# Performance work log

Hardware: AMD Instinct MI355X
Metric: run time of the kernel (lower is better)

The kernel has to match this reference:

```python
import jax, jax.numpy as jnp
import numpy as np

N_TOKEN = 267735
CUTS = [0, 20000, 40000, 200000, 267735]
DIV = 4
D_MODEL = 1024
N_HEAD = 16
D_HEAD = 64
D_INNER = 4096
N_LAYER = 4
QLEN = 512
MLEN = 512
BSZ = 4
EPS = 1e-5


def _ln(x, g, b):
    mu = jnp.mean(x, axis=-1, keepdims=True)
    var = jnp.var(x, axis=-1, keepdims=True)
    return (x - mu) * jax.lax.rsqrt(var + EPS) * g + b


def _rel_shift(x):
    # x: [qlen, klen, bsz, n_head]
    q, k, b, n = x.shape
    x = jnp.pad(x, ((0, 0), (1, 0), (0, 0), (0, 0)))
    x = x.reshape(k + 1, q, b, n)[1:]
    return x.reshape(q, k, b, n)


def setup_inputs() -> dict:
    key = jax.random.key(0)
    ks = list(jax.random.split(key, 32))
    p = lambda i, shape: 0.02 * jax.random.normal(ks[i], shape, dtype=jnp.float32)
    inp = {}
    inp['input_ids'] = jax.random.randint(ks[0], (BSZ, QLEN), 0, N_TOKEN, dtype=jnp.int32)
    inp['mems'] = 0.05 * jax.random.normal(ks[1], (N_LAYER, MLEN, BSZ, D_MODEL), dtype=jnp.float32)
    # adaptive embedding: cluster tables + projections (div_val=4)
    for i in range(4):
        l, r = CUTS[i], CUTS[i + 1]
        d_i = D_MODEL // (DIV ** i)
        inp[f'emb{i}'] = p(2 + i, (r - l, d_i))
        inp[f'proj{i}'] = p(6 + i, (d_i, D_MODEL))
    H = N_HEAD * D_HEAD
    inp['qkv_W'] = p(10, (N_LAYER, D_MODEL, 3 * H))
    inp['r_W'] = p(11, (N_LAYER, D_MODEL, H))
    inp['o_W'] = p(12, (N_LAYER, H, D_MODEL))
    inp['r_w_bias'] = p(13, (N_LAYER, N_HEAD, D_HEAD))
    inp['r_r_bias'] = p(14, (N_LAYER, N_HEAD, D_HEAD))
    inp['ln1_g'] = jnp.ones((N_LAYER, D_MODEL), jnp.float32)
    inp['ln1_b'] = jnp.zeros((N_LAYER, D_MODEL), jnp.float32)
    inp['ff_w1'] = p(15, (N_LAYER, D_MODEL, D_INNER))
    inp['ff_b1'] = jnp.zeros((N_LAYER, D_INNER), jnp.float32)
    inp['ff_w2'] = p(16, (N_LAYER, D_INNER, D_MODEL))
    inp['ff_b2'] = jnp.zeros((N_LAYER, D_MODEL), jnp.float32)
    inp['ln2_g'] = jnp.ones((N_LAYER, D_MODEL), jnp.float32)
    inp['ln2_b'] = jnp.zeros((N_LAYER, D_MODEL), jnp.float32)
    return inp


def _forward(input_ids, mems, embs, projs, qkv_W, r_W, o_W, r_w_bias, r_r_bias,
             ln1_g, ln1_b, ff_w1, ff_b1, ff_w2, ff_b2, ln2_g, ln2_b):
    ids = input_ids.T  # [qlen, bsz]
    qlen, bsz = ids.shape
    mems = jax.lax.stop_gradient(mems)  # mems are detached in the original
    mlen = mems.shape[1]
    klen = qlen + mlen

    # --- adaptive embedding (masked gather + scatter-add, same math as boolean_mask/scatter_nd) ---
    flat = ids.reshape(-1)
    emb = jnp.zeros((flat.shape[0], D_MODEL), jnp.float32)
    for i in range(4):
        l, r = CUTS[i], CUTS[i + 1]
        mask = (flat >= l) & (flat < r)
        idx = jnp.clip(flat - l, 0, r - l - 1)
        e_i = jnp.einsum('id,de->ie', embs[i][idx], projs[i])
        emb = emb + jnp.where(mask[:, None], e_i, 0.0)
    word_emb = (emb * (D_MODEL ** 0.5)).reshape(qlen, bsz, D_MODEL)

    # --- sinusoidal relative positions, pos_seq = klen-1 .. 0 ---
    pos_seq = jnp.arange(klen - 1, -1, -1, dtype=jnp.float32)
    inv_freq = 1.0 / (10000.0 ** (jnp.arange(0, D_MODEL, 2, dtype=jnp.float32) / D_MODEL))
    sinusoid = jnp.einsum('i,j->ij', pos_seq, inv_freq)
    pos_emb = jnp.concatenate([jnp.sin(sinusoid), jnp.cos(sinusoid)], axis=-1)  # [klen, d_model]

    # causal mask over memory-extended keys: [qlen, klen]
    attn_mask = jnp.triu(jnp.ones((qlen, klen), jnp.float32), k=1 + mlen)
    mask4 = attn_mask[:, :, None, None]
    scale = 1.0 / (D_HEAD ** 0.5)

    h = word_emb
    for l in range(N_LAYER):
        cat = jnp.concatenate([mems[l], h], axis=0)  # [klen, bsz, d_model]
        w_heads = jnp.einsum('kbd,dh->kbh', cat, qkv_W[l])
        r_head_k = jnp.einsum('kd,dh->kh', pos_emb, r_W[l]).reshape(klen, N_HEAD, D_HEAD)
        q_h, k_h, v_h = jnp.split(w_heads, 3, axis=-1)
        q_h = q_h[-qlen:].reshape(qlen, bsz, N_HEAD, D_HEAD)
        k_h = k_h.reshape(klen, bsz, N_HEAD, D_HEAD)
        v_h = v_h.reshape(klen, bsz, N_HEAD, D_HEAD)
        AC = jnp.einsum('ibnd,jbnd->ijbn', q_h + r_w_bias[l], k_h)
        BD = _rel_shift(jnp.einsum('ibnd,jnd->ijbn', q_h + r_r_bias[l], r_head_k))
        score = (AC + BD) * scale
        score = score * (1.0 - mask4) - 1e30 * mask4
        prob = jax.nn.softmax(score, axis=1)
        attn_vec = jnp.einsum('ijbn,jbnd->ibnd', prob, v_h).reshape(qlen, bsz, N_HEAD * D_HEAD)
        attn_out = jnp.einsum('ibh,hd->ibd', attn_vec, o_W[l])
        h = _ln(h + attn_out, ln1_g[l], ln1_b[l])
        ff = jnp.einsum('ibf,fd->ibd', jax.nn.relu(jnp.einsum('ibd,df->ibf', h, ff_w1[l]) + ff_b1[l]), ff_w2[l]) + ff_b2[l]
        h = _ln(h + ff, ln2_g[l], ln2_b[l])

    return h.transpose(1, 0, 2)  # [bsz, qlen, d_model]


def reference(input_ids, mems, emb0, emb1, emb2, emb3, proj0, proj1, proj2, proj3,
              qkv_W, r_W, o_W, r_w_bias, r_r_bias, ln1_g, ln1_b,
              ff_w1, ff_b1, ff_w2, ff_b2, ln2_g, ln2_b):
    return _forward(input_ids, mems, (emb0, emb1, emb2, emb3), (proj0, proj1, proj2, proj3),
                    qkv_W, r_W, o_W, r_w_bias, r_r_bias, ln1_g, ln1_b,
                    ff_w1, ff_b1, ff_w2, ff_b2, ln2_g, ln2_b)
```

## Files before the change

kernel.cpp:

```cpp
#include <hip/hip_runtime.h>

typedef __attribute__((ext_vector_type(8))) short bf16x8;
typedef __attribute__((ext_vector_type(4))) float f32x4;

#define N_LAYER 4
#define QLEN 512
#define MLEN 512
#define KLEN 1024
#define BSZ 4
#define DM 1024
#define NH 16
#define DH 64
#define DINNER 4096
#define EK 1408
#define BDLD 1152

__device__ __forceinline__ unsigned short f2bf(float x) {
    unsigned u = __float_as_uint(x);
    u += 0x7fffu + ((u >> 16) & 1u);
    return (unsigned short)(u >> 16);
}
__device__ __forceinline__ float bf2f(unsigned short v) {
    return __uint_as_float(((unsigned)v) << 16);
}

__device__ __forceinline__ void gload16(const unsigned short* g, unsigned short* l) {
    __builtin_amdgcn_global_load_lds(
        (const __attribute__((address_space(1))) unsigned int*)g,
        (__attribute__((address_space(3))) unsigned int*)l, 16, 0, 0);
}

__device__ __forceinline__ bf16x8 lds_read8_sw(const unsigned short* base, int row, int cb) {
    return *(const bf16x8*)((const char*)base + row * 128 + (cb ^ ((row & 7) << 4)));
}

__global__ __launch_bounds__(256)
void transpose_all(const float* __restrict__ qkvWl, const float* __restrict__ rWl,
                   const float* __restrict__ oWl, const float* __restrict__ w1l,
                   const float* __restrict__ w2l,
                   unsigned short* __restrict__ qkvT, unsigned short* __restrict__ rT,
                   unsigned short* __restrict__ oT, unsigned short* __restrict__ w1T,
                   unsigned short* __restrict__ w2T) {
    __shared__ float tile[64][65];
    int id = blockIdx.x;
    const float* W; unsigned short* D; int K, N, bx, by;
    if (id < 768)       { W = qkvWl; D = qkvT; K = 1024; N = 3072; bx = id % 48; by = id / 48; }
    else if (id < 1024) { id -= 768;  W = rWl;  D = rT;  K = 1024; N = 1024; bx = id & 15; by = id >> 4; }
    else if (id < 1280) { id -= 1024; W = oWl;  D = oT;  K = 1024; N = 1024; bx = id & 15; by = id >> 4; }
    else if (id < 2304) { id -= 1280; W = w1l;  D = w1T; K = 1024; N = 4096; bx = id & 63; by = id >> 6; }
    else                { id -= 2304; W = w2l;  D = w2T; K = 4096; N = 1024; bx = id & 15; by = id >> 4; }
    const int tid = threadIdx.x;
#pragma unroll
    for (int s = 0; s < 4; ++s) {
        int idx = s * 256 + tid;
        int kr = idx >> 4, c4 = (idx & 15) * 4;
        float4 v = *(const float4*)(W + (size_t)(by * 64 + kr) * N + bx * 64 + c4);
        tile[kr][c4] = v.x; tile[kr][c4 + 1] = v.y;
        tile[kr][c4 + 2] = v.z; tile[kr][c4 + 3] = v.w;
    }
    __syncthreads();
#pragma unroll
    for (int s = 0; s < 2; ++s) {
        int idx = s * 256 + tid;
        int nl = idx >> 3, k8 = (idx & 7) * 8;
        unsigned short tmp[8];
#pragma unroll
        for (int j = 0; j < 8; ++j) tmp[j] = f2bf(tile[k8 + j][nl]);
        *(uint4*)(D + (size_t)(bx * 64 + nl) * K + by * 64 + k8) = *(uint4*)tmp;
    }
}

__global__ __launch_bounds__(256)
void transpose_pad(const float* __restrict__ W, unsigned short* __restrict__ dst,
                   int K, int N, int dstLD, int dstOff) {
    __shared__ float tile[32][33];
    const int tx = threadIdx.x & 31, ty = threadIdx.x >> 5;
    const int bx = blockIdx.x, by = blockIdx.y;
#pragma unroll
    for (int i = 0; i < 4; ++i) {
        int k = by * 32 + ty + i * 8;
        tile[ty + i * 8][tx] = (k < K) ? W[(size_t)k * N + bx * 32 + tx] : 0.f;
    }
    __syncthreads();
#pragma unroll
    for (int i = 0; i < 4; ++i) {
        int n = bx * 32 + ty + i * 8;
        int k = by * 32 + tx;
        dst[(size_t)n * dstLD + dstOff + k] = f2bf(tile[tx][ty + i * 8]);
    }
}

__global__ __launch_bounds__(256)
void emb_gather(const int* __restrict__ ids,
                const float* __restrict__ e0, const float* __restrict__ e1,
                const float* __restrict__ e2, const float* __restrict__ e3,
                unsigned short* __restrict__ embA) {
    const int chunk = blockIdx.x * 256 + threadIdx.x;
    if (chunk >= 2048 * 176) return;
    const int t = chunk / 176;
    const int e8 = (chunk - t * 176) * 8;
    const int i = t >> 2, b = t & 3;
    const int id = ids[b * QLEN + i];
    const float* src = nullptr;
    if (e8 < 1024) {
        if (id < 20000) src = e0 + (size_t)id * 1024 + e8;
    } else if (e8 < 1280) {
        if (id >= 20000 && id < 40000) src = e1 + (size_t)(id - 20000) * 256 + (e8 - 1024);
    } else if (e8 < 1344) {
        if (id >= 40000 && id < 200000) src = e2 + (size_t)(id - 40000) * 64 + (e8 - 1280);
    } else if (e8 < 1360) {
        if (id >= 200000) src = e3 + (size_t)(id - 200000) * 16 + (e8 - 1344);
    }
    uint4 o = {0u, 0u, 0u, 0u};
    if (src) {
        float4 v0 = *(const float4*)src;
        float4 v1 = *(const float4*)(src + 4);
        o.x = (unsigned)f2bf(v0.x * 32.f) | ((unsigned)f2bf(v0.y * 32.f) << 16);
        o.y = (unsigned)f2bf(v0.z * 32.f) | ((unsigned)f2bf(v0.w * 32.f) << 16);
        o.z = (unsigned)f2bf(v1.x * 32.f) | ((unsigned)f2bf(v1.y * 32.f) << 16);
        o.w = (unsigned)f2bf(v1.z * 32.f) | ((unsigned)f2bf(v1.w * 32.f) << 16);
    }
    *(uint4*)(embA + (size_t)t * EK + e8) = o;
}

template <int MODE, int BN>
__global__ __launch_bounds__(256)
void gemm_bt(const unsigned short* __restrict__ A, const unsigned short* __restrict__ BT,
             float* __restrict__ C, unsigned short* __restrict__ Cbf,
             const float* __restrict__ bias, int M, int N, int K) {
    constexpr int NF = BN / 32;
    __shared__ unsigned short lA[2][128 * 64];
    __shared__ unsigned short lB[2][BN * 64];
    const int tid = threadIdx.x;
    const int w = tid >> 6, l = tid & 63;
    const int lane15 = l & 15, lh = l >> 4;
    const int nwg = gridDim.x;
    const int cpx = nwg >> 3;
    const int swz = (blockIdx.x & 7) * cpx + (blockIdx.x >> 3);
    const int nbn = N / BN;
    const int bm = swz / nbn, bn = swz % nbn;
    const int wr = (w >> 1) * 64, wc = (w & 1) * (BN / 2);

    f32x4 acc[4][NF] = {};

    const unsigned short* gA = A + (size_t)(bm * 128) * K;
    const unsigned short* gB = BT + (size_t)(bn * BN) * K;

    auto stage = [&](int buf, int k0) {
#pragma unroll
        for (int s = 0; s < 4; ++s) {
            int g = tid + s * 256, row = g >> 3;
            gload16(gA + (size_t)row * K + k0 + ((g & 7) ^ (row & 7)) * 8,
                    lA[buf] + g * 8);
        }
#pragma unroll
        for (int s = 0; s < BN / 32; ++s) {
            int g = tid + s * 256, row = g >> 3;
            gload16(gB + (size_t)row * K + k0 + ((g & 7) ^ (row & 7)) * 8,
                    lB[buf] + g * 8);
        }
    };

    stage(0, 0);
    __syncthreads();
    int cur = 0;
    for (int k0 = 0; k0 < K; k0 += 64) {
        if (k0 + 64 < K) stage(cur ^ 1, k0 + 64);
        const unsigned short* cA = lA[cur];
        const unsigned short* cB = lB[cur];
#pragma unroll
        for (int kk = 0; kk < 2; ++kk) {
            bf16x8 af[4], bfr[NF];
#pragma unroll
            for (int f = 0; f < 4; ++f)
                af[f] = lds_read8_sw(cA, wr + f * 16 + lane15, kk * 64 + lh * 16);
#pragma unroll
            for (int f = 0; f < NF; ++f)
                bfr[f] = lds_read8_sw(cB, wc + f * 16 + lane15, kk * 64 + lh * 16);
#pragma unroll
            for (int mi = 0; mi < 4; ++mi)
#pragma unroll
                for (int ni = 0; ni < NF; ++ni)
                    acc[mi][ni] = __builtin_amdgcn_mfma_f32_16x16x32_bf16(
                        af[mi], bfr[ni], acc[mi][ni], 0, 0, 0);
        }
        __syncthreads();
        cur ^= 1;
    }

#pragma unroll
    for (int mi = 0; mi < 4; ++mi) {
        int rowb = bm * 128 + wr + mi * 16 + lh * 4;
#pragma unroll
        for (int ni = 0; ni < NF; ++ni) {
            int col = bn * BN + wc + ni * 16 + lane15;
#pragma unroll
            for (int r = 0; r < 4; ++r) {
                float x = acc[mi][ni][r];
                if (MODE == 0) {
                    C[(size_t)(rowb + r) * N + col] = x;
                } else if (MODE == 1) {
                    x += bias[col];
                    Cbf[(size_t)(rowb + r) * N + col] = f2bf(x > 0.f ? x : 0.f);
                } else if (MODE == 2) {
                    C[(size_t)(rowb + r) * N + col] = x + bias[col];
                } else {
                    C[(size_t)(rowb + r) * N + col] = x;
                    Cbf[(size_t)(rowb + r) * N + col] = f2bf(x);
                }
            }
        }
    }
}

__global__ __launch_bounds__(256)
void qkv_rk_gemm(const unsigned short* __restrict__ catb, const unsigned short* __restrict__ posb,
                 const unsigned short* __restrict__ qkvT, const unsigned short* __restrict__ rT,
                 const float* __restrict__ rwb, const float* __restrict__ rrb,
                 unsigned short* __restrict__ Qw, unsigned short* __restrict__ Qr,
                 unsigned short* __restrict__ Kb, unsigned short* __restrict__ VTb,
                 unsigned short* __restrict__ Rb) {
    __shared__ unsigned short lA[2][128 * 64];
    __shared__ unsigned short lB[2][128 * 64];
    const int tid = threadIdx.x;
    const int w = tid >> 6, l = tid & 63;
    const int lane15 = l & 15, lh = l >> 4;
    const int cpx = gridDim.x >> 3;
    const int swz = (blockIdx.x & 7) * cpx + (blockIdx.x >> 3);
    const int wr = (w >> 1) * 64, wc = (w & 1) * 64;

    const unsigned short* gA;
    const unsigned short* gB;
    int part, bm, bn;
    if (swz < 512)      { part = 0; bm = swz >> 4; bn = swz & 15;
                          gA = catb + (size_t)(bm * 128) * 1024;
                          gB = qkvT + (size_t)(1024 + bn * 128) * 1024; }
    else if (swz < 640) { part = 1; int q = swz - 512; bm = q >> 3; bn = q & 7;
                          gA = catb + (size_t)(2048 + bm * 128) * 1024;
                          gB = qkvT + (size_t)(bn * 128) * 1024; }
    else                { part = 2; int q = swz - 640; bm = q >> 3; bn = q & 7;
                          gA = posb + (size_t)(bm * 128) * 1024;
                          gB = rT + (size_t)(bn * 128) * 1024; }

    f32x4 acc[4][4] = {};
    auto stage = [&](int buf, int k0) {
#pragma unroll
        for (int s = 0; s < 4; ++s) {
            int g = tid + s * 256, row = g >> 3;
            gload16(gA + (size_t)row * 1024 + k0 + ((g & 7) ^ (row & 7)) * 8, lA[buf] + g * 8);
            gload16(gB + (size_t)row * 1024 + k0 + ((g & 7) ^ (row & 7)) * 8, lB[buf] + g * 8);
        }
    };
    stage(0, 0);
    __syncthreads();
    int cur = 0;
    for (int k0 = 0; k0 < 1024; k0 += 64) {
        if (k0 + 64 < 1024) stage(cur ^ 1, k0 + 64);
        const unsigned short* cA = lA[cur];
        const unsigned short* cB = lB[cur];
#pragma unroll
        for (int kk = 0; kk < 2; ++kk) {
            bf16x8 af[4], bfr[4];
#pragma unroll
            for (int f = 0; f < 4; ++f) {
                af[f]  = lds_read8_sw(cA, wr + f * 16 + lane15, kk * 64 + lh * 16);
                bfr[f] = lds_read8_sw(cB, wc + f * 16 + lane15, kk * 64 + lh * 16);
            }
#pragma unroll
            for (int mi = 0; mi < 4; ++mi)
#pragma unroll
                for (int ni = 0; ni < 4; ++ni)
                    acc[mi][ni] = __builtin_amdgcn_mfma_f32_16x16x32_bf16(
                        af[mi], bfr[ni], acc[mi][ni], 0, 0, 0);
        }
        __syncthreads();
        cur ^= 1;
    }

#pragma unroll
    for (int mi = 0; mi < 4; ++mi) {
        int rowb = bm * 128 + wr + mi * 16 + lh * 4;
#pragma unroll
        for (int ni = 0; ni < 4; ++ni) {
            int col = bn * 128 + wc + ni * 16 + lane15;
#pragma unroll
            for (int r = 0; r < 4; ++r) {
                float x = acc[mi][ni][r];
                if (part == 0) {
                    int j = rowb >> 2, bb_ = r;
                    if (col < 1024) {
                        int n = col >> 6, d = col & 63;
                        Kb[((size_t)(bb_ * NH + n) * KLEN + j) * DH + d] = f2bf(x);
                    } else {
                        int c2 = col - 1024, n = c2 >> 6, d = c2 & 63;
                        VTb[((size_t)(bb_ * NH + n) * DH + d) * KLEN + j] = f2bf(x);
                    }
                } else if (part == 1) {
                    int i = rowb >> 2, bb_ = r;
                    int n = col >> 6, d = col & 63;
                    size_t o = ((size_t)(bb_ * NH + n) * QLEN + i) * DH + d;
                    Qw[o] = f2bf((x + rwb[col]) * 0.125f);
                    Qr[o] = f2bf(x + rrb[col]);
                } else {
                    int j = rowb + r;
                    int n = col >> 6, d = col & 63;
                    Rb[((size_t)n * KLEN + j) * DH + d] = f2bf(x);
                }
            }
        }
    }
}

__global__ __launch_bounds__(256)
void bd_gemm(const unsigned short* __restrict__ Qr, const unsigned short* __restrict__ Rb,
             unsigned short* __restrict__ BDs) {
    __shared__ unsigned short lA[128 * 64];
    __shared__ unsigned short lB[128 * 64];
    const int tid = threadIdx.x;
    const int w = tid >> 6, l = tid & 63;
    const int lane15 = l & 15, lh = l >> 4;
    const int blk = blockIdx.x;
    const int bn = blk & 63;
    const int tile = blk >> 6;
    const int bd_mi[26] = {0,0,0,0,0, 1,1,1,1,1,1, 2,2,2,2,2,2,2, 3,3,3,3,3,3,3,3};
    const int bd_nj[26] = {3,4,5,6,7, 2,3,4,5,6,7, 1,2,3,4,5,6,7, 0,1,2,3,4,5,6,7};
    const int mi_ = bd_mi[tile], nj = bd_nj[tile];
    const int n = bn & 15;
    const int wr = (w >> 1) * 64, wc = (w & 1) * 64;

    const unsigned short* gA = Qr + (size_t)bn * QLEN * DH + (size_t)(mi_ * 128) * 64;
    const unsigned short* gB = Rb + (size_t)n * KLEN * DH + (size_t)(nj * 128) * 64;
#pragma unroll
    for (int s = 0; s < 4; ++s) {
        int g = tid + s * 256, row = g >> 3;
        gload16(gA + (size_t)row * 64 + ((g & 7) ^ (row & 7)) * 8, lA + g * 8);
        gload16(gB + (size_t)row * 64 + ((g & 7) ^ (row & 7)) * 8, lB + g * 8);
    }
    __syncthreads();
    f32x4 acc[4][4] = {};
#pragma unroll
    for (int kk = 0; kk < 2; ++kk) {
        bf16x8 af[4], bfr[4];
#pragma unroll
        for (int f = 0; f < 4; ++f) {
            af[f]  = lds_read8_sw(lA, wr + f * 16 + lane15, kk * 64 + lh * 16);
            bfr[f] = lds_read8_sw(lB, wc + f * 16 + lane15, kk * 64 + lh * 16);
        }
#pragma unroll
        for (int mi = 0; mi < 4; ++mi)
#pragma unroll
            for (int ni = 0; ni < 4; ++ni)
                acc[mi][ni] = __builtin_amdgcn_mfma_f32_16x16x32_bf16(
                    af[mi], bfr[ni], acc[mi][ni], 0, 0, 0);
    }
    unsigned short* out = BDs + (size_t)bn * 512 * BDLD;
#pragma unroll
    for (int mi = 0; mi < 4; ++mi) {
        int rowb = mi_ * 128 + wr + mi * 16 + lh * 4;
#pragma unroll
        for (int ni = 0; ni < 4; ++ni) {
            int col = nj * 128 + wc + ni * 16 + lane15;
#pragma unroll
            for (int r = 0; r < 4; ++r)
                out[(size_t)(rowb + r) * BDLD + col] = f2bf(acc[mi][ni][r] * 0.125f);
        }
    }
}

__global__ __launch_bounds__(256)
void pos_kernel(unsigned short* __restrict__ posbf) {
    const int p = blockIdx.x, tid = threadIdx.x;
    const float ps = (float)(KLEN - 1 - p);
    const float c = -2.0f * 9.210340371976184f / 1024.0f;
#pragma unroll
    for (int j4 = 0; j4 < 4; ++j4) {
        int j = tid + j4 * 256;
        int m = (j < 512) ? j : j - 512;
        float freq = __expf((float)m * c);
        float ang = ps * freq;
        float v = (j < 512) ? sinf(ang) : cosf(ang);
        posbf[(size_t)p * DM + j] = f2bf(v);
    }
}

__global__ __launch_bounds__(256)
void mems_cat(const float* __restrict__ mem_l, unsigned short* __restrict__ catbf) {
    const int t = blockIdx.x, tid = threadIdx.x;
    float4 v = ((const float4*)(mem_l + (size_t)t * DM))[tid];
    uint2 o;
    o.x = (unsigned)f2bf(v.x) | ((unsigned)f2bf(v.y) << 16);
    o.y = (unsigned)f2bf(v.z) | ((unsigned)f2bf(v.w) << 16);
    ((uint2*)(catbf + (size_t)t * DM))[tid] = o;
}

__global__ __launch_bounds__(64)
void attn_part(const unsigned short* __restrict__ Qw,
               const unsigned short* __restrict__ Kb, const unsigned short* __restrict__ VTb,
               const unsigned short* __restrict__ BDs,
               unsigned short* __restrict__ Opart, float* __restrict__ ms) {
    __shared__ unsigned short lP[16 * 64];

    const int l = threadIdx.x;
    const int lane15 = l & 15, lh = l >> 4;
    const int blk = blockIdx.x;
    const int bn = blk & 63;
    const int rest = blk >> 6;
    const int rg = rest & 3;
    const int c = rest >> 2;

    const int offt[8] = {0, 3, 7, 11, 15, 20, 25, 30};
    const int nctt[8] = {3, 4, 4, 4, 5, 5, 5, 6};
    int it = 0;
#pragma unroll
    for (int i = 1; i < 8; ++i) if (c >= offt[i]) it = i;
    const int cl = c - offt[it];
    const int nck = nctt[it];
    const int ntiles = it + 9;
    const int jt0 = (cl * ntiles) / nck;
    const int jt1 = ((cl + 1) * ntiles) / nck;
    const int i0 = it * 64;
    const int rowl = rg * 16 + lh * 4;

    bf16x8 qw[2];
    {
        size_t qb = ((size_t)bn * QLEN + i0 + rg * 16 + lane15) * DH + lh * 8;
        qw[0] = *(const bf16x8*)(Qw + qb);
        qw[1] = *(const bf16x8*)(Qw + qb + 32);
    }
    bf16x8 onesb;
#pragma unroll
    for (int j = 0; j < 8; ++j) onesb[j] = (short)0x3F80;

    const unsigned short* kp = Kb + (size_t)bn * KLEN * DH + (size_t)(jt0 * 64 + lane15) * DH + lh * 8;
    const unsigned short* vp = VTb + (size_t)bn * DH * KLEN + (size_t)lane15 * KLEN + jt0 * 64 + lh * 8;
    const unsigned short* bdp[4];
#pragma unroll
    for (int r = 0; r < 4; ++r) {
        int row = i0 + rowl + r;
        bdp[r] = BDs + (size_t)bn * 512 * BDLD + (size_t)row * BDLD
                 + (511 - row) + jt0 * 64 + lane15;
    }

    f32x4 oacc[4] = {};
    f32x4 srowv = {};

    for (int jt = jt0; jt < jt1; ++jt) {
        float bdv[4][4];
#pragma unroll
        for (int f = 0; f < 4; ++f)
#pragma unroll
            for (int r = 0; r < 4; ++r)
                bdv[f][r] = bf2f(bdp[r][16 * f]);

        bf16x8 kf[2][4];
#pragma unroll
        for (int f = 0; f < 4; ++f) {
            const unsigned short* p = kp + (size_t)(f * 16) * DH;
            kf[0][f] = *(const bf16x8*)p;
            kf[1][f] = *(const bf16x8*)(p + 32);
        }

        f32x4 sac[4] = {};
        __builtin_amdgcn_s_setprio(1);
#pragma unroll
        for (int kk = 0; kk < 2; ++kk)
#pragma unroll
            for (int f = 0; f < 4; ++f)
                sac[f] = __builtin_amdgcn_mfma_f32_16x16x32_bf16(qw[kk], kf[kk][f], sac[f], 0, 0, 0);
        __builtin_amdgcn_s_setprio(0);

        bf16x8 vf[2][4];
#pragma unroll
        for (int kk = 0; kk < 2; ++kk)
#pragma unroll
            for (int f = 0; f < 4; ++f)
                vf[kk][f] = *(const bf16x8*)(vp + (size_t)(f * 16) * KLEN + kk * 32);

        const bool lastTile = (jt == it + 8);
        float pv[4][4];
#pragma unroll
        for (int f = 0; f < 4; ++f) {
            int lj = lane15 + 16 * f;
#pragma unroll
            for (int r = 0; r < 4; ++r) {
                float s = sac[f][r] + bdv[f][r];
                if (lastTile && (lj > rowl + r)) s = -1e30f;
                pv[f][r] = __expf(s - 8.f);
            }
        }

#pragma unroll
        for (int f = 0; f < 4; ++f)
#pragma unroll
            for (int r = 0; r < 4; ++r) {
                int row = lh * 4 + r, cb2 = (lane15 + 16 * f) * 2;
                *(unsigned short*)((char*)lP + row * 128 + (cb2 ^ ((row & 7) << 4))) =
                    f2bf(pv[f][r]);
            }
        bf16x8 pa[2];
        pa[0] = lds_read8_sw(lP, lane15, lh * 16);
        pa[1] = lds_read8_sw(lP, lane15, 64 + lh * 16);

        __builtin_amdgcn_s_setprio(1);
#pragma unroll
        for (int kk = 0; kk < 2; ++kk) {
#pragma unroll
            for (int f = 0; f < 4; ++f)
                oacc[f] = __builtin_amdgcn_mfma_f32_16x16x32_bf16(pa[kk], vf[kk][f], oacc[f], 0, 0, 0);
            srowv = __builtin_amdgcn_mfma_f32_16x16x32_bf16(pa[kk], onesb, srowv, 0, 0, 0);
        }
        __builtin_amdgcn_s_setprio(0);

        kp += 64 * DH;
        vp += 64;
#pragma unroll
        for (int r = 0; r < 4; ++r) bdp[r] += 64;
    }

    const int slot = (bn * 8 + it) * 6 + cl;
    unsigned short* Op = Opart + (size_t)slot * 4096;
#pragma unroll
    for (int f = 0; f < 4; ++f)
#pragma unroll
        for (int r = 0; r < 4; ++r)
            Op[(rowl + r) * 64 + lane15 + 16 * f] = f2bf(oacc[f][r]);
    if (lane15 == 0) {
        float* msp = ms + (size_t)slot * 64;
#pragma unroll
        for (int r = 0; r < 4; ++r) msp[rowl + r] = srowv[r];
    }
}

__global__ __launch_bounds__(256)
void attn_merge(const unsigned short* __restrict__ Opart, const float* __restrict__ ms,
                unsigned short* __restrict__ avec) {
    const int blk = blockIdx.x;
    const int bn = blk & 63, it = blk >> 6;
    const int n = bn & 15, b = bn >> 4;
    const int nctt[8] = {3, 4, 4, 4, 5, 5, 5, 6};
    const int k = nctt[it];
    const int tid = threadIdx.x;
    const int r = tid >> 2, cq = (tid & 3) * 16;
    const int base_slot = (bn * 8 + it) * 6;

    float S = 0.f;
    for (int c = 0; c < k; ++c) S += ms[(size_t)(base_slot + c) * 64 + r];

    float acc[16];
#pragma unroll
    for (int j = 0; j < 16; ++j) acc[j] = 0.f;
    for (int c = 0; c < k; ++c) {
        const bf16x8* op = (const bf16x8*)(Opart + (size_t)(base_slot + c) * 4096 + r * 64 + cq);
        bf16x8 v0 = op[0], v1 = op[1];
#pragma unroll
        for (int j = 0; j < 8; ++j) {
            acc[j]     += bf2f((unsigned short)v0[j]);
            acc[8 + j] += bf2f((unsigned short)v1[j]);
        }
    }
    float inv = 1.0f / S;
    int t = (it * 64 + r) * 4 + b;
    unsigned short* dst = avec + (size_t)t * DM + n * 64 + cq;
#pragma unroll
    for (int j = 0; j < 16; ++j) dst[j] = f2bf(acc[j] * inv);
}

__global__ __launch_bounds__(256)
void ln_kernel(const float* __restrict__ hin, const float* __restrict__ res,
               const float* __restrict__ g, const float* __restrict__ bb,
               float* __restrict__ hout, unsigned short* __restrict__ hbf) {
    __shared__ float ls[8];
    const int t = blockIdx.x, tid = threadIdx.x;
    float4 x = ((const float4*)(hin + (size_t)t * DM))[tid];
    float4 rr = ((const float4*)(res + (size_t)t * DM))[tid];
    float v0 = x.x + rr.x, v1 = x.y + rr.y, v2 = x.z + rr.z, v3 = x.w + rr.w;
    float s = v0 + v1 + v2 + v3;
    float sq = v0 * v0 + v1 * v1 + v2 * v2 + v3 * v3;
#pragma unroll
    for (int off = 1; off < 64; off <<= 1) {
        s += __shfl_xor(s, off);
        sq += __shfl_xor(sq, off);
    }
    const int w = tid >> 6;
    if ((tid & 63) == 0) { ls[w] = s; ls[4 + w] = sq; }
    __syncthreads();
    s = ls[0] + ls[1] + ls[2] + ls[3];
    sq = ls[4] + ls[5] + ls[6] + ls[7];
    float mu = s * (1.f / 1024.f);
    float var = sq * (1.f / 1024.f) - mu * mu;
    float rstd = rsqrtf(var + 1e-5f);
    float y[4] = {v0, v1, v2, v3};
    float4 of;
    uint2 ob;
    float* op = &of.x;
#pragma unroll
    for (int j = 0; j < 4; ++j) {
        int d = tid * 4 + j;
        op[j] = (y[j] - mu) * rstd * g[d] + bb[d];
    }
    ob.x = (unsigned)f2bf(of.x) | ((unsigned)f2bf(of.y) << 16);
    ob.y = (unsigned)f2bf(of.z) | ((unsigned)f2bf(of.w) << 16);
    ((float4*)(hout + (size_t)t * DM))[tid] = of;
    ((uint2*)(hbf + (size_t)t * DM))[tid] = ob;
}

__global__ __launch_bounds__(256)
void out_kernel(const float* __restrict__ h, float* __restrict__ out) {
    const int t = blockIdx.x, tid = threadIdx.x;
    const int i = t >> 2, b = t & 3;
    ((float4*)(out + ((size_t)b * QLEN + i) * DM))[tid] =
        ((const float4*)(h + (size_t)t * DM))[tid];
}

extern "C" void kernel_launch(void* const* d_in, const int* in_sizes, int n_in,
                              void* d_out, int out_size, void* d_ws, size_t ws_size,
                              hipStream_t stream) {
    const int* ids = (const int*)d_in[0];
    const float* mems = (const float*)d_in[1];
    const float* embp[4] = {nullptr, nullptr, nullptr, nullptr};
    const float* projp[4] = {nullptr, nullptr, nullptr, nullptr};
    const long long esz[4] = {20000LL * 1024, 20000LL * 256, 160000LL * 64, 67735LL * 16};
    const long long psz[4] = {1024LL * 1024, 256LL * 1024, 64LL * 1024, 16LL * 1024};
    for (int idx = 2; idx <= 9 && idx < n_in; ++idx) {
        long long s = in_sizes[idx];
        for (int c = 0; c < 4; ++c) {
            if (s == esz[c]) embp[c] = (const float*)d_in[idx];
            else if (s == psz[c]) projp[c] = (const float*)d_in[idx];
        }
    }
    const float* qkvW = (const float*)d_in[10];
    const float* rW   = (const float*)d_in[11];
    const float* oW   = (const float*)d_in[12];
    const float* rwb  = (const float*)d_in[13];
    const float* rrb  = (const float*)d_in[14];
    const float* ln1g = (const float*)d_in[15];
    const float* ln1b = (const float*)d_in[16];
    const float* ffw1 = (const float*)d_in[17];
    const float* ffb1 = (const float*)d_in[18];
    const float* ffw2 = (const float*)d_in[19];
    const float* ffb2 = (const float*)d_in[20];
    const float* ln2g = (const float*)d_in[21];
    const float* ln2b = (const float*)d_in[22];

    size_t off = 0;
    char* base = (char*)d_ws;
    auto alloc = [&](size_t bytes) -> char* {
        char* p = base + off;
        off = (off + bytes + 255) & ~(size_t)255;
        return p;
    };
    unsigned short* qkvT  = (unsigned short*)alloc(3072ull * 1024 * 2);
    unsigned short* rT    = (unsigned short*)alloc(1024ull * 1024 * 2);
    unsigned short* oT    = (unsigned short*)alloc(1024ull * 1024 * 2);
    unsigned short* w1T   = (unsigned short*)alloc(4096ull * 1024 * 2);
    unsigned short* w2T   = (unsigned short*)alloc(1024ull * 4096 * 2);
    unsigned short* embA  = (unsigned short*)alloc(2048ull * EK * 2);
    unsigned short* embBT = (unsigned short*)alloc(1024ull * EK * 2);
    float* h              = (float*)alloc(2048ull * 1024 * 4);
    unsigned short* hbf   = (unsigned short*)alloc(2048ull * 1024 * 2);
    unsigned short* catb  = (unsigned short*)alloc(4096ull * 1024 * 2);
    unsigned short* posb  = (unsigned short*)alloc(1024ull * 1024 * 2);
    unsigned short* Qw    = (unsigned short*)alloc(4ull * 16 * 512 * 64 * 2);
    unsigned short* Qr    = (unsigned short*)alloc(4ull * 16 * 512 * 64 * 2);
    unsigned short* Kb    = (unsigned short*)alloc(4ull * 16 * 1024 * 64 * 2);
    unsigned short* VTb   = (unsigned short*)alloc(4ull * 16 * 1024 * 64 * 2);
    unsigned short* Rb    = (unsigned short*)alloc(16ull * 1024 * 64 * 2);
    unsigned short* avec  = (unsigned short*)alloc(2048ull * 1024 * 2);
    float* resid          = (float*)alloc(2048ull * 1024 * 4);
    unsigned short* ff1b  = (unsigned short*)alloc(2048ull * 4096 * 2);
    unsigned short* Opart = (unsigned short*)alloc(3072ull * 4096 * 2);
    float* msbuf          = (float*)alloc(3072ull * 64 * 4);
    unsigned short* BDs   = (unsigned short*)alloc(64ull * 512 * BDLD * 2);
    (void)ws_size; (void)out_size;

    unsigned short* catbHi = catb + 2048ull * 1024;

    emb_gather<<<(2048 * 176 + 255) / 256, 256, 0, stream>>>(
        ids, embp[0], embp[1], embp[2], embp[3], embA);
    transpose_pad<<<dim3(32, 32), 256, 0, stream>>>(projp[0], embBT, 1024, 1024, EK, 0);
    transpose_pad<<<dim3(32, 8),  256, 0, stream>>>(projp[1], embBT, 256,  1024, EK, 1024);
    transpose_pad<<<dim3(32, 2),  256, 0, stream>>>(projp[2], embBT, 64,   1024, EK, 1280);
    transpose_pad<<<dim3(32, 2),  256, 0, stream>>>(projp[3], embBT, 16,   1024, EK, 1344);
    pos_kernel<<<1024, 256, 0, stream>>>(posb);
    gemm_bt<5, 128><<<(2048 / 128) * (1024 / 128), 256, 0, stream>>>(
        embA, embBT, h, catbHi, nullptr, 2048, 1024, EK);

    for (int l = 0; l < N_LAYER; ++l) {
        const float* qkvWl = qkvW + (size_t)l * 1024 * 3072;
        const float* rWl   = rW + (size_t)l * 1024 * 1024;
        const float* oWl   = oW + (size_t)l * 1024 * 1024;
        const float* w1l   = ffw1 + (size_t)l * 1024 * 4096;
        const float* w2l   = ffw2 + (size_t)l * 4096 * 1024;

        transpose_all<<<3328, 256, 0, stream>>>(qkvWl, rWl, oWl, w1l, w2l,
                                                qkvT, rT, oT, w1T, w2T);

        mems_cat<<<2048, 256, 0, stream>>>(mems + (size_t)l * 2048 * 1024, catb);

        qkv_rk_gemm<<<704, 256, 0, stream>>>(catb, posb, qkvT, rT,
                                             rwb + l * 1024, rrb + l * 1024,
                                             Qw, Qr, Kb, VTb, Rb);

        bd_gemm<<<64 * 26, 256, 0, stream>>>(Qr, Rb, BDs);

        attn_part<<<64 * 144, 64, 0, stream>>>(Qw, Kb, VTb, BDs, Opart, msbuf);
        attn_merge<<<512, 256, 0, stream>>>(Opart, msbuf, avec);

        gemm_bt<0, 64><<<(2048 / 128) * (1024 / 64), 256, 0, stream>>>(
            avec, oT, resid, nullptr, nullptr, 2048, 1024, 1024);
        ln_kernel<<<2048, 256, 0, stream>>>(h, resid, ln1g + l * 1024, ln1b + l * 1024, h, hbf);

        gemm_bt<1, 128><<<(2048 / 128) * (4096 / 128), 256, 0, stream>>>(
            hbf, w1T, nullptr, ff1b, ffb1 + l * 4096, 2048, 4096, 1024);
        gemm_bt<2, 64><<<(2048 / 128) * (1024 / 64), 256, 0, stream>>>(
            ff1b, w2T, resid, nullptr, ffb2 + l * 1024, 2048, 1024, 4096);
        ln_kernel<<<2048, 256, 0, stream>>>(h, resid, ln2g + l * 1024, ln2b + l * 1024, h,
                                            (l < 3) ? catbHi : hbf);
    }

    out_kernel<<<2048, 256, 0, stream>>>(h, (float*)d_out);
}
```

Baseline: 1.078 ms.

## Split-K the output-projection and FF2 GEMMs and fold the partial sums into layernorm

```diff
diff --git a/kernel.cpp b/kernel.cpp
--- a/kernel.cpp
+++ b/kernel.cpp
@@ -209,6 +209,89 @@
                     Cbf[(size_t)(rowb + r) * N + col] = f2bf(x);
                 }
             }
+        }
+    }
+}
+
+template <int BN>
+__global__ __launch_bounds__(256)
+void gemm_sk(const unsigned short* __restrict__ A, const unsigned short* __restrict__ BT,
+             float* __restrict__ C01, int M, int N, int K) {
+    constexpr int NF = BN / 32;
+    __shared__ unsigned short lA[2][128 * 64];
+    __shared__ unsigned short lB[2][BN * 64];
+    const int tid = threadIdx.x;
+    const int w = tid >> 6, l = tid & 63;
+    const int lane15 = l & 15, lh = l >> 4;
+    const int nwg = gridDim.x;
+    const int cpx = nwg >> 3;
+    const int swz = (blockIdx.x & 7) * cpx + (blockIdx.x >> 3);
+    const int nbn = N / BN;
+    const int nhalf = (M / 128) * nbn;
+    const int half = swz / nhalf;
+    const int rem = swz % nhalf;
+    const int bm = rem / nbn, bn = rem % nbn;
+    const int KH = K >> 1;
+    const int koff = half * KH;
+    const int wr = (w >> 1) * 64, wc = (w & 1) * (BN / 2);
+
+    f32x4 acc[4][NF] = {};
+
+    const unsigned short* gA = A + (size_t)(bm * 128) * K + koff;
+    const unsigned short* gB = BT + (size_t)(bn * BN) * K + koff;
+
+    auto stage = [&](int buf, int k0) {
+#pragma unroll
+        for (int s = 0; s < 4; ++s) {
+            int g = tid + s * 256, row = g >> 3;
+            gload16(gA + (size_t)row * K + k0 + ((g & 7) ^ (row & 7)) * 8,
+                    lA[buf] + g * 8);
+        }
+#pragma unroll
+        for (int s = 0; s < BN / 32; ++s) {
+            int g = tid + s * 256, row = g >> 3;
+            gload16(gB + (size_t)row * K + k0 + ((g & 7) ^ (row & 7)) * 8,
+                    lB[buf] + g * 8);
+        }
+    };
+
+    stage(0, 0);
+    __syncthreads();
+    int cur = 0;
+    for (int k0 = 0; k0 < KH; k0 += 64) {
+        if (k0 + 64 < KH) stage(cur ^ 1, k0 + 64);
+        const unsigned short* cA = lA[cur];
+        const unsigned short* cB = lB[cur];
+#pragma unroll
+        for (int kk = 0; kk < 2; ++kk) {
+            bf16x8 af[4], bfr[NF];
+#pragma unroll
+            for (int f = 0; f < 4; ++f)
+                af[f] = lds_read8_sw(cA, wr + f * 16 + lane15, kk * 64 + lh * 16);
+#pragma unroll
+            for (int f = 0; f < NF; ++f)
+                bfr[f] = lds_read8_sw(cB, wc + f * 16 + lane15, kk * 64 + lh * 16);
+#pragma unroll
+            for (int mi = 0; mi < 4; ++mi)
+#pragma unroll
+                for (int ni = 0; ni < NF; ++ni)
+                    acc[mi][ni] = __builtin_amdgcn_mfma_f32_16x16x32_bf16(
+                        af[mi], bfr[ni], acc[mi][ni], 0, 0, 0);
+        }
+        __syncthreads();
+        cur ^= 1;
+    }
+
+    float* Cout = C01 + (size_t)half * M * N;
+#pragma unroll
+    for (int mi = 0; mi < 4; ++mi) {
+        int rowb = bm * 128 + wr + mi * 16 + lh * 4;
+#pragma unroll
+        for (int ni = 0; ni < NF; ++ni) {
+            int col = bn * BN + wc + ni * 16 + lane15;
+#pragma unroll
+            for (int r = 0; r < 4; ++r)
+                Cout[(size_t)(rowb + r) * N + col] = acc[mi][ni][r];
         }
     }
 }
@@ -566,14 +649,21 @@
 }
 
 __global__ __launch_bounds__(256)
-void ln_kernel(const float* __restrict__ hin, const float* __restrict__ res,
+void ln_kernel(const float* __restrict__ hin, const float* __restrict__ res0,
+               const float* __restrict__ res1, const float* __restrict__ bias2,
                const float* __restrict__ g, const float* __restrict__ bb,
                float* __restrict__ hout, unsigned short* __restrict__ hbf) {
     __shared__ float ls[8];
     const int t = blockIdx.x, tid = threadIdx.x;
     float4 x = ((const float4*)(hin + (size_t)t * DM))[tid];
-    float4 rr = ((const float4*)(res + (size_t)t * DM))[tid];
-    float v0 = x.x + rr.x, v1 = x.y + rr.y, v2 = x.z + rr.z, v3 = x.w + rr.w;
+    float4 r0 = ((const float4*)(res0 + (size_t)t * DM))[tid];
+    float4 r1 = ((const float4*)(res1 + (size_t)t * DM))[tid];
+    float v0 = x.x + r0.x + r1.x, v1 = x.y + r0.y + r1.y;
+    float v2 = x.z + r0.z + r1.z, v3 = x.w + r0.w + r1.w;
+    if (bias2) {
+        float4 b2 = ((const float4*)bias2)[tid];
+        v0 += b2.x; v1 += b2.y; v2 += b2.z; v3 += b2.w;
+    }
     float s = v0 + v1 + v2 + v3;
     float sq = v0 * v0 + v1 * v1 + v2 * v2 + v3 * v3;
 #pragma unroll
@@ -666,7 +756,7 @@
     unsigned short* VTb   = (unsigned short*)alloc(4ull * 16 * 1024 * 64 * 2);
     unsigned short* Rb    = (unsigned short*)alloc(16ull * 1024 * 64 * 2);
     unsigned short* avec  = (unsigned short*)alloc(2048ull * 1024 * 2);
-    float* resid          = (float*)alloc(2048ull * 1024 * 4);
+    float* resid01        = (float*)alloc(2ull * 2048 * 1024 * 4);
     unsigned short* ff1b  = (unsigned short*)alloc(2048ull * 4096 * 2);
     unsigned short* Opart = (unsigned short*)alloc(3072ull * 4096 * 2);
     float* msbuf          = (float*)alloc(3072ull * 64 * 4);
@@ -674,6 +764,7 @@
     (void)ws_size; (void)out_size;
 
     unsigned short* catbHi = catb + 2048ull * 1024;
+    float* resid1 = resid01 + 2048ull * 1024;
 
     emb_gather<<<(2048 * 176 + 255) / 256, 256, 0, stream>>>(
         ids, embp[0], embp[1], embp[2], embp[3], embA);
@@ -706,15 +797,18 @@
         attn_part<<<64 * 144, 64, 0, stream>>>(Qw, Kb, VTb, BDs, Opart, msbuf);
         attn_merge<<<512, 256, 0, stream>>>(Opart, msbuf, avec);
 
-        gemm_bt<0, 64><<<(2048 / 128) * (1024 / 64), 256, 0, stream>>>(
-            avec, oT, resid, nullptr, nullptr, 2048, 1024, 1024);
-        ln_kernel<<<2048, 256, 0, stream>>>(h, resid, ln1g + l * 1024, ln1b + l * 1024, h, hbf);
+        gemm_sk<64><<<2 * (2048 / 128) * (1024 / 64), 256, 0, stream>>>(
+            avec, oT, resid01, 2048, 1024, 1024);
+        ln_kernel<<<2048, 256, 0, stream>>>(h, resid01, resid1, nullptr,
+                                            ln1g + l * 1024, ln1b + l * 1024, h, hbf);
 
         gemm_bt<1, 128><<<(2048 / 128) * (4096 / 128), 256, 0, stream>>>(
             hbf, w1T, nullptr, ff1b, ffb1 + l * 4096, 2048, 4096, 1024);
-        gemm_bt<2, 64><<<(2048 / 128) * (1024 / 64), 256, 0, stream>>>(
-            ff1b, w2T, resid, nullptr, ffb2 + l * 1024, 2048, 1024, 4096);
-        ln_kernel<<<2048, 256, 0, stream>>>(h, resid, ln2g + l * 1024, ln2b + l * 1024, h,
+
+        gemm_sk<64><<<2 * (2048 / 128) * (1024 / 64), 256, 0, stream>>>(
+            ff1b, w2T, resid01, 2048, 1024, 4096);
+        ln_kernel<<<2048, 256, 0, stream>>>(h, resid01, resid1, ffb2 + l * 1024,
+                                            ln2g + l * 1024, ln2b + l * 1024, h,
                                             (l < 3) ? catbHi : hbf);
     }
 
```

Result: faster. 975.4 us (-9.5%).
